# Optimization experiments

Measured on AMD Instinct MI355X. Metric: run time of the kernel, lower is better.

## Reference

```python
import jax, jax.numpy as jnp
import numpy as np

B, T, C = 2, 2048, 2048
H, HKV, D = 16, 4, 128
GROUPS = H // HKV  # num_key_value_groups
EPS = 1e-6


def setup_inputs() -> dict:
    key = jax.random.key(0)
    ks = jax.random.split(key, 6)
    s = 0.02
    return {
        "hidden_states": jax.random.normal(ks[0], (B, T, C), jnp.float32),
        "Wq": jax.random.normal(ks[1], (C, H * D), jnp.float32) * s,
        "Wk": jax.random.normal(ks[2], (C, HKV * D), jnp.float32) * s,
        "Wv": jax.random.normal(ks[3], (C, HKV * D), jnp.float32) * s,
        "Wo": jax.random.normal(ks[4], (H * D, C), jnp.float32) * s,
        "keep_mask": jax.random.randint(ks[5], (T,), 0, 2) > 0,
    }


def reference(hidden_states, Wq, Wk, Wv, Wo, keep_mask):
    # Base attention (standard causal GQA attention with output_attentions=True)
    q = (hidden_states @ Wq).reshape(B, T, H, D).transpose(0, 2, 1, 3)      # [B,H,T,D]
    k = (hidden_states @ Wk).reshape(B, T, HKV, D).transpose(0, 2, 1, 3)    # [B,Hkv,S,D]
    v = (hidden_states @ Wv).reshape(B, T, HKV, D).transpose(0, 2, 1, 3)    # [B,Hkv,S,D]
    k_rep = jnp.repeat(k, GROUPS, axis=1)                                    # [B,H,S,D]
    v_rep = jnp.repeat(v, GROUPS, axis=1)                                    # [B,H,S,D]
    scale = 1.0 / jnp.sqrt(jnp.float32(D))
    scores = jnp.einsum("bhtd,bhsd->bhts", q, k_rep) * scale                 # [B,H,T,S]
    causal = jnp.tril(jnp.ones((T, T), dtype=bool))
    scores = jnp.where(causal[None, None], scores, jnp.float32(-1e9))
    attn_w = jax.nn.softmax(scores, axis=-1)                                 # [B,H,T,S]

    # ScratchpadPrunedAttention: mask dropped positions, renormalize,
    # recompute context and o_proj.
    keep = keep_mask.astype(attn_w.dtype)[None, None, None, :]               # [1,1,1,S]
    attn_w = attn_w * keep
    attn_w = attn_w / (attn_w.sum(-1, keepdims=True) + EPS)
    new_ctx = jnp.einsum("bhts,bhsd->bhtd", attn_w, v_rep)                   # [B,H,T,D]
    new_ctx = new_ctx.transpose(0, 2, 1, 3).reshape(B, T, H * D)             # [B,T,H*D]
    out = new_ctx @ Wo                                                        # [B,T,C]
    return out, attn_w
```

## Files before the change

### kernel.cpp

```cpp
#include <hip/hip_runtime.h>
#include <hip/hip_bf16.h>
#include <stdint.h>

#define B_ 2
#define T_ 2048
#define C_ 2048
#define H_ 16
#define HKV_ 4
#define D_ 128
#define M_ (B_*T_)
static constexpr float SCL = 0.08838834764831845f * 1.4426950408889634f;
static constexpr float EPS_ = 1e-6f;

typedef short bf16x8 __attribute__((ext_vector_type(8)));
typedef float f32x4 __attribute__((ext_vector_type(4)));

__device__ __forceinline__ f32x4 zero4() {
  f32x4 v; v[0] = 0.f; v[1] = 0.f; v[2] = 0.f; v[3] = 0.f; return v;
}

__device__ __forceinline__ unsigned short f2bf(float x) {
  union { float f; unsigned u; } v; v.f = x;
  unsigned r = (v.u + 0x7FFFu + ((v.u >> 16) & 1u)) >> 16;
  return (unsigned short)r;
}

__device__ __forceinline__ void gl_lds16(const void* g, void* l) {
  __builtin_amdgcn_global_load_lds((const __attribute__((address_space(1))) void*)g,
                                   (__attribute__((address_space(3))) void*)l, 16, 0, 0);
}

__global__ void k_cvt(const float* __restrict__ in, unsigned short* __restrict__ out, int n) {
  int i = (blockIdx.x * blockDim.x + threadIdx.x) * 8;
  int stride = gridDim.x * blockDim.x * 8;
  for (; i < n; i += stride) {
    float4 a = *(const float4*)(in + i);
    float4 b = *(const float4*)(in + i + 4);
    ushort4 o0; o0.x = f2bf(a.x); o0.y = f2bf(a.y); o0.z = f2bf(a.z); o0.w = f2bf(a.w);
    ushort4 o1; o1.x = f2bf(b.x); o1.y = f2bf(b.y); o1.z = f2bf(b.z); o1.w = f2bf(b.w);
    *(ushort4*)(out + i) = o0;
    *(ushort4*)(out + i + 4) = o1;
  }
}

__global__ void k_cvt_t(const float* __restrict__ in, unsigned short* __restrict__ out,
                        int R, int Cc) {
  __shared__ float ld[32][33];
  int c0 = blockIdx.x * 32, r0 = blockIdx.y * 32;
  int x = threadIdx.x, y = threadIdx.y;
#pragma unroll
  for (int i = 0; i < 4; i++)
    ld[y * 4 + i][x] = in[(size_t)(r0 + y * 4 + i) * Cc + c0 + x];
  __syncthreads();
#pragma unroll
  for (int i = 0; i < 4; i++)
    out[(size_t)(c0 + y * 4 + i) * R + r0 + x] = f2bf(ld[x][y * 4 + i]);
}

template <int WRITE_F32>
__global__ __launch_bounds__(256) void k_gemm(const unsigned short* __restrict__ A,
                                              const unsigned short* __restrict__ Bt,
                                              void* __restrict__ Cout,
                                              int Mdim, int Ndim, int K) {
  __shared__ __align__(16) unsigned short As[128 * 64];
  __shared__ __align__(16) unsigned short Bs[128 * 64];
  const int tid = threadIdx.x;
  const int wid = tid >> 6, lane = tid & 63;
  const int wm = wid >> 1, wn = wid & 1;
  const int m0 = blockIdx.y * 128, n0 = blockIdx.x * 128;
  const int lrow = tid >> 3, lcol = (tid & 7) * 8;
  const int g = lane >> 4, lr = lane & 15;

  f32x4 acc[4][4];
#pragma unroll
  for (int i = 0; i < 4; i++)
#pragma unroll
    for (int j = 0; j < 4; j++) acc[i][j] = zero4();

  for (int k0 = 0; k0 < K; k0 += 64) {
    __syncthreads();
#pragma unroll
    for (int it = 0; it < 4; it++) {
      gl_lds16(A + (size_t)(m0 + lrow + it * 32) * K + k0 + lcol, (void*)(As + tid * 8 + it * 2048));
      gl_lds16(Bt + (size_t)(n0 + lrow + it * 32) * K + k0 + lcol, (void*)(Bs + tid * 8 + it * 2048));
    }
    __syncthreads();
#pragma unroll
    for (int kk = 0; kk < 2; kk++) {
      bf16x8 af[4], bfr[4];
#pragma unroll
      for (int i = 0; i < 4; i++)
        af[i] = *(const bf16x8*)(As + (wm * 64 + i * 16 + lr) * 64 + kk * 32 + g * 8);
#pragma unroll
      for (int j = 0; j < 4; j++)
        bfr[j] = *(const bf16x8*)(Bs + (wn * 64 + j * 16 + lr) * 64 + kk * 32 + g * 8);
#pragma unroll
      for (int i = 0; i < 4; i++)
#pragma unroll
        for (int j = 0; j < 4; j++)
          acc[i][j] = __builtin_amdgcn_mfma_f32_16x16x32_bf16(af[i], bfr[j], acc[i][j], 0, 0, 0);
    }
  }

#pragma unroll
  for (int i = 0; i < 4; i++)
#pragma unroll
    for (int j = 0; j < 4; j++)
#pragma unroll
      for (int r = 0; r < 4; r++) {
        int row = m0 + wm * 64 + i * 16 + g * 4 + r;
        int col = n0 + wn * 64 + j * 16 + lr;
        if (WRITE_F32)
          ((float*)Cout)[(size_t)row * Ndim + col] = acc[i][j][r];
        else
          ((unsigned short*)Cout)[(size_t)row * Ndim + col] = f2bf(acc[i][j][r]);
      }
}

__global__ __launch_bounds__(256) void k_attn(const unsigned short* __restrict__ qb,
                                              const unsigned short* __restrict__ kb,
                                              const unsigned short* __restrict__ vt,
                                              const int* __restrict__ mask,
                                              float* __restrict__ attn,
                                              unsigned short* __restrict__ ctx)
{
  __shared__ __align__(16) unsigned short Ks[2][64 * 128];
  __shared__ __align__(16) unsigned short Vs[2][128 * 64];
  __shared__ __align__(16) unsigned short Ps[4][16 * 64];
  __shared__ float keeps[2048];

  const int tid = threadIdx.x;
  const int wid = tid >> 6, lane = tid & 63;
  const int g = lane >> 4, lr = lane & 15;
  const int lr7 = lr & 7;
  const int qt = 31 - blockIdx.y;
  const int bh = blockIdx.x;
  const int b = bh >> 4, h = bh & 15, hkv = h >> 2;
  const int qbase = qt * 64;

  const unsigned short* qp = qb + (size_t)(b * T_ + qbase) * 2048 + h * 128;
  const unsigned short* kp = kb + (size_t)(b * T_) * 512 + hkv * 128;
  const unsigned short* vp = vt + (size_t)(hkv * 128) * 4096 + b * T_;
  float* ap = attn + (size_t)(bh * T_ + qbase) * 2048;
  unsigned short* cp = ctx + (size_t)(b * T_ + qbase) * 2048 + h * 128;

#pragma unroll
  for (int i = 0; i < 8; i++)
    keeps[tid * 8 + i] = (mask[tid * 8 + i] != 0) ? 1.0f : 0.0f;

  bf16x8 qa[4];
#pragma unroll
  for (int ks = 0; ks < 4; ks++)
    qa[ks] = *(const bf16x8*)(qp + (size_t)(wid * 16 + lr) * 2048 + ks * 32 + g * 8);

  const int srow = tid >> 4;
  const int scolb = ((tid & 15) * 16) ^ ((srow & 7) << 4);
  const int vrow = tid >> 3;
  const int vcolb = ((tid & 7) * 16) ^ ((vrow & 7) << 4);

  auto stageK = [&](int st, int bufi) {
    const unsigned short* src = kp + (size_t)(st * 64 + srow) * 512 + (scolb >> 1);
    unsigned short* dst = Ks[bufi] + tid * 8;
#pragma unroll
    for (int it = 0; it < 4; it++)
      gl_lds16(src + (size_t)it * 16 * 512, (void*)(dst + it * 2048));
  };
  auto stageV = [&](int st, int bufi) {
    const unsigned short* src = vp + (size_t)vrow * 4096 + st * 64 + (vcolb >> 1);
    unsigned short* dst = Vs[bufi] + tid * 8;
#pragma unroll
    for (int it = 0; it < 4; it++)
      gl_lds16(src + (size_t)it * 32 * 4096, (void*)(dst + it * 2048));
  };

  float z[4] = {0, 0, 0, 0}, zk[4] = {0, 0, 0, 0};

  stageK(0, 0);
  asm volatile("s_waitcnt vmcnt(0) lgkmcnt(0)" ::: "memory");
  __builtin_amdgcn_s_barrier();
  for (int st = 0; st <= qt; st++) {
    const int cur = st & 1;
    if (st < qt) stageK(st + 1, cur ^ 1);
    const unsigned short* kt = Ks[cur];
#pragma unroll
    for (int j = 0; j < 4; j++) {
      f32x4 sc = zero4();
      const unsigned short* kbase = kt + (j * 16 + lr) * 128;
#pragma unroll
      for (int ks = 0; ks < 4; ks++) {
        bf16x8 kf = *(const bf16x8*)(kbase + (((ks * 64 + g * 16) ^ (lr7 << 4)) >> 1));
        sc = __builtin_amdgcn_mfma_f32_16x16x32_bf16(qa[ks], kf, sc, 0, 0, 0);
      }
      int sg = st * 64 + j * 16 + lr;
      float kpv = keeps[sg];
#pragma unroll
      for (int r = 0; r < 4; r++) {
        int tg = qbase + wid * 16 + g * 4 + r;
        float e = (sg <= tg) ? __builtin_amdgcn_exp2f(sc[r] * SCL) : 0.0f;
        z[r] += e;
        zk[r] += e * kpv;
      }
    }
    asm volatile("s_waitcnt vmcnt(0)" ::: "memory");
    __builtin_amdgcn_s_barrier();
  }

  stageK(qt, 0);
  stageV(qt, 0);
#pragma unroll
  for (int r = 0; r < 4; r++) {
#pragma unroll
    for (int m = 1; m < 16; m <<= 1) {
      z[r] += __shfl_xor(z[r], m);
      zk[r] += __shfl_xor(zk[r], m);
    }
  }
  float inv[4];
#pragma unroll
  for (int r = 0; r < 4; r++) inv[r] = 1.0f / (zk[r] + EPS_ * z[r]);

  f32x4 cacc[8];
#pragma unroll
  for (int n = 0; n < 8; n++) cacc[n] = zero4();

  asm volatile("s_waitcnt vmcnt(0)" ::: "memory");
  __builtin_amdgcn_s_barrier();

  for (int st = qt; st >= 0; st--) {
    const int cur = (qt - st) & 1;
    if (st > 0) { stageK(st - 1, cur ^ 1); stageV(st - 1, cur ^ 1); }
    __builtin_amdgcn_sched_barrier(0);
    const int s0 = st * 64;
    const unsigned short* kt = Ks[cur];
    const unsigned short* vtile = Vs[cur];
#pragma unroll
    for (int j = 0; j < 4; j++) {
      f32x4 sc = zero4();
      const unsigned short* kbase = kt + (j * 16 + lr) * 128;
#pragma unroll
      for (int ks = 0; ks < 4; ks++) {
        bf16x8 kf = *(const bf16x8*)(kbase + (((ks * 64 + g * 16) ^ (lr7 << 4)) >> 1));
        sc = __builtin_amdgcn_mfma_f32_16x16x32_bf16(qa[ks], kf, sc, 0, 0, 0);
      }
      int sg = s0 + j * 16 + lr;
      float kpv = keeps[sg];
#pragma unroll
      for (int r = 0; r < 4; r++) {
        int row = wid * 16 + g * 4 + r;
        int tg = qbase + row;
        float e = (sg <= tg) ? __builtin_amdgcn_exp2f(sc[r] * SCL) : 0.0f;
        float a = e * kpv * inv[r];
        ap[(size_t)row * 2048 + sg] = a;
        int prow = g * 4 + r;
        Ps[wid][prow * 64 + (((j * 32 + lr * 2) ^ ((prow & 7) << 4)) >> 1)] = f2bf(a);
      }
    }
    asm volatile("s_waitcnt lgkmcnt(0)" ::: "memory");
    __builtin_amdgcn_sched_barrier(0);
#pragma unroll
    for (int kk = 0; kk < 2; kk++) {
      bf16x8 pa = *(const bf16x8*)(&Ps[wid][lr * 64 + (((kk * 64 + g * 16) ^ (lr7 << 4)) >> 1)]);
#pragma unroll
      for (int n = 0; n < 8; n++) {
        bf16x8 vf = *(const bf16x8*)(vtile + (n * 16 + lr) * 64 + (((kk * 64 + g * 16) ^ (lr7 << 4)) >> 1));
        cacc[n] = __builtin_amdgcn_mfma_f32_16x16x32_bf16(pa, vf, cacc[n], 0, 0, 0);
      }
    }
    asm volatile("s_waitcnt vmcnt(16)" ::: "memory");
    __builtin_amdgcn_s_barrier();
  }

#pragma unroll
  for (int n = 0; n < 8; n++)
#pragma unroll
    for (int r = 0; r < 4; r++)
      cp[(size_t)(wid * 16 + g * 4 + r) * 2048 + n * 16 + lr] = f2bf(cacc[n][r]);

  const int zc0 = qbase + 64;
  if (zc0 < 2048) {
    float4 zf; zf.x = 0.f; zf.y = 0.f; zf.z = 0.f; zf.w = 0.f;
    float* aprow = ap + (size_t)(tid >> 2) * 2048;
    for (int c = zc0 + (tid & 3) * 4; c < 2048; c += 16)
      *(float4*)(aprow + c) = zf;
  }
}

extern "C" void kernel_launch(void* const* d_in, const int* in_sizes, int n_in,
                              void* d_out, int out_size, void* d_ws, size_t ws_size,
                              hipStream_t stream) {
  const float* hs = (const float*)d_in[0];
  const float* Wq = (const float*)d_in[1];
  const float* Wk = (const float*)d_in[2];
  const float* Wv = (const float*)d_in[3];
  const float* Wo = (const float*)d_in[4];
  const int* mask = (const int*)d_in[5];

  char* w = (char*)d_ws;
  unsigned short* hsb = (unsigned short*)w; w += (size_t)M_ * C_ * 2;
  unsigned short* Wqt = (unsigned short*)w; w += (size_t)2048 * 2048 * 2;
  unsigned short* Wkt = (unsigned short*)w; w += (size_t)512 * 2048 * 2;
  unsigned short* Wvt = (unsigned short*)w; w += (size_t)512 * 2048 * 2;
  unsigned short* Wot = (unsigned short*)w; w += (size_t)2048 * 2048 * 2;
  unsigned short* qbuf = (unsigned short*)w; w += (size_t)M_ * 2048 * 2;
  unsigned short* kbuf = (unsigned short*)w; w += (size_t)M_ * 512 * 2;
  unsigned short* vtb = (unsigned short*)w; w += (size_t)512 * M_ * 2;
  unsigned short* ctxb = (unsigned short*)w; w += (size_t)M_ * 2048 * 2;

  float* out = (float*)d_out;
  float* attn = out + (size_t)M_ * C_;

  k_cvt<<<2048, 256, 0, stream>>>(hs, hsb, M_ * C_);
  k_cvt_t<<<dim3(2048 / 32, 2048 / 32), dim3(32, 8), 0, stream>>>(Wq, Wqt, 2048, 2048);
  k_cvt_t<<<dim3(512 / 32, 2048 / 32), dim3(32, 8), 0, stream>>>(Wk, Wkt, 2048, 512);
  k_cvt_t<<<dim3(512 / 32, 2048 / 32), dim3(32, 8), 0, stream>>>(Wv, Wvt, 2048, 512);
  k_cvt_t<<<dim3(2048 / 32, 2048 / 32), dim3(32, 8), 0, stream>>>(Wo, Wot, 2048, 2048);

  k_gemm<0><<<dim3(2048 / 128, 4096 / 128), 256, 0, stream>>>(hsb, Wqt, qbuf, 4096, 2048, 2048);
  k_gemm<0><<<dim3(512 / 128, 4096 / 128), 256, 0, stream>>>(hsb, Wkt, kbuf, 4096, 512, 2048);
  k_gemm<0><<<dim3(4096 / 128, 512 / 128), 256, 0, stream>>>(Wvt, hsb, vtb, 512, 4096, 2048);

  k_attn<<<dim3(32, 32), 256, 0, stream>>>(qbuf, kbuf, vtb, mask, attn, ctxb);

  k_gemm<1><<<dim3(2048 / 128, 4096 / 128), 256, 0, stream>>>(ctxb, Wot, out, 4096, 2048, 2048);
}
```

Measured before the change: 462.9 us.

## Halve attention KV tile to 32, pack keep mask into bits, raise occupancy

Shrinks the attention kernel's K/V staging tiles from 64 to 32 keys, which cuts LDS use so more blocks fit per CU, and adds a launch bound of 4 blocks per CU. The per-block float keep array in LDS is replaced by a tiny pre-kernel that packs the mask into 32-bit words, read per tile. s_setprio hints are placed around the MFMA sections and the vmcnt wait is adjusted to the smaller staging count. In exchange there are twice as many loop iterations and barriers per block, plus one extra tiny kernel launch.

```diff
diff --git a/kernel.cpp b/kernel.cpp
--- a/kernel.cpp
+++ b/kernel.cpp
@@ -55,6 +55,16 @@
 #pragma unroll
   for (int i = 0; i < 4; i++)
     out[(size_t)(c0 + y * 4 + i) * R + r0 + x] = f2bf(ld[x][y * 4 + i]);
+}
+
+__global__ void k_maskbits(const int* __restrict__ mask, unsigned int* __restrict__ mb) {
+  int t = threadIdx.x;
+  if (t < 64) {
+    unsigned int w = 0;
+    for (int b = 0; b < 32; b++)
+      if (mask[t * 32 + b] != 0) w |= (1u << b);
+    mb[t] = w;
+  }
 }
 
 template <int WRITE_F32>
@@ -117,26 +127,26 @@
       }
 }
 
-__global__ __launch_bounds__(256) void k_attn(const unsigned short* __restrict__ qb,
-                                              const unsigned short* __restrict__ kb,
-                                              const unsigned short* __restrict__ vt,
-                                              const int* __restrict__ mask,
-                                              float* __restrict__ attn,
-                                              unsigned short* __restrict__ ctx)
+__global__ __launch_bounds__(256, 4) void k_attn(const unsigned short* __restrict__ qb,
+                                                 const unsigned short* __restrict__ kb,
+                                                 const unsigned short* __restrict__ vt,
+                                                 const unsigned int* __restrict__ mb,
+                                                 float* __restrict__ attn,
+                                                 unsigned short* __restrict__ ctx)
 {
-  __shared__ __align__(16) unsigned short Ks[2][64 * 128];
-  __shared__ __align__(16) unsigned short Vs[2][128 * 64];
-  __shared__ __align__(16) unsigned short Ps[4][16 * 64];
-  __shared__ float keeps[2048];
+  __shared__ __align__(16) unsigned short Ks[2][32 * 128];
+  __shared__ __align__(16) unsigned short Vs[2][128 * 32];
+  __shared__ __align__(16) unsigned short Ps[4][16 * 32];
 
   const int tid = threadIdx.x;
   const int wid = tid >> 6, lane = tid & 63;
   const int g = lane >> 4, lr = lane & 15;
-  const int lr7 = lr & 7;
+  const int lr7 = lr & 7, lr3 = lr & 3;
   const int qt = 31 - blockIdx.y;
   const int bh = blockIdx.x;
   const int b = bh >> 4, h = bh & 15, hkv = h >> 2;
   const int qbase = qt * 64;
+  const int ntile = 2 * qt + 2;
 
   const unsigned short* qp = qb + (size_t)(b * T_ + qbase) * 2048 + h * 128;
   const unsigned short* kp = kb + (size_t)(b * T_) * 512 + hkv * 128;
@@ -144,10 +154,6 @@
   float* ap = attn + (size_t)(bh * T_ + qbase) * 2048;
   unsigned short* cp = ctx + (size_t)(b * T_ + qbase) * 2048 + h * 128;
 
-#pragma unroll
-  for (int i = 0; i < 8; i++)
-    keeps[tid * 8 + i] = (mask[tid * 8 + i] != 0) ? 1.0f : 0.0f;
-
   bf16x8 qa[4];
 #pragma unroll
   for (int ks = 0; ks < 4; ks++)
@@ -155,22 +161,22 @@
 
   const int srow = tid >> 4;
   const int scolb = ((tid & 15) * 16) ^ ((srow & 7) << 4);
-  const int vrow = tid >> 3;
-  const int vcolb = ((tid & 7) * 16) ^ ((vrow & 7) << 4);
+  const int vrow = tid >> 2;
+  const int vcolb = ((tid & 3) * 16) ^ ((vrow & 3) << 4);
 
   auto stageK = [&](int st, int bufi) {
-    const unsigned short* src = kp + (size_t)(st * 64 + srow) * 512 + (scolb >> 1);
+    const unsigned short* src = kp + (size_t)(st * 32 + srow) * 512 + (scolb >> 1);
     unsigned short* dst = Ks[bufi] + tid * 8;
 #pragma unroll
-    for (int it = 0; it < 4; it++)
+    for (int it = 0; it < 2; it++)
       gl_lds16(src + (size_t)it * 16 * 512, (void*)(dst + it * 2048));
   };
   auto stageV = [&](int st, int bufi) {
-    const unsigned short* src = vp + (size_t)vrow * 4096 + st * 64 + (vcolb >> 1);
+    const unsigned short* src = vp + (size_t)vrow * 4096 + st * 32 + (vcolb >> 1);
     unsigned short* dst = Vs[bufi] + tid * 8;
 #pragma unroll
-    for (int it = 0; it < 4; it++)
-      gl_lds16(src + (size_t)it * 32 * 4096, (void*)(dst + it * 2048));
+    for (int it = 0; it < 2; it++)
+      gl_lds16(src + (size_t)it * 64 * 4096, (void*)(dst + it * 2048));
   };
 
   float z[4] = {0, 0, 0, 0}, zk[4] = {0, 0, 0, 0};
@@ -178,21 +184,24 @@
   stageK(0, 0);
   asm volatile("s_waitcnt vmcnt(0) lgkmcnt(0)" ::: "memory");
   __builtin_amdgcn_s_barrier();
-  for (int st = 0; st <= qt; st++) {
+  for (int st = 0; st < ntile; st++) {
     const int cur = st & 1;
-    if (st < qt) stageK(st + 1, cur ^ 1);
+    if (st + 1 < ntile) stageK(st + 1, cur ^ 1);
     const unsigned short* kt = Ks[cur];
 #pragma unroll
-    for (int j = 0; j < 4; j++) {
+    for (int j = 0; j < 2; j++) {
       f32x4 sc = zero4();
       const unsigned short* kbase = kt + (j * 16 + lr) * 128;
+      __builtin_amdgcn_s_setprio(1);
 #pragma unroll
       for (int ks = 0; ks < 4; ks++) {
         bf16x8 kf = *(const bf16x8*)(kbase + (((ks * 64 + g * 16) ^ (lr7 << 4)) >> 1));
         sc = __builtin_amdgcn_mfma_f32_16x16x32_bf16(qa[ks], kf, sc, 0, 0, 0);
       }
-      int sg = st * 64 + j * 16 + lr;
-      float kpv = keeps[sg];
+      __builtin_amdgcn_s_setprio(0);
+      int sg = st * 32 + j * 16 + lr;
+      unsigned int w = mb[st];
+      float kpv = (float)((w >> (j * 16 + lr)) & 1u);
 #pragma unroll
       for (int r = 0; r < 4; r++) {
         int tg = qbase + wid * 16 + g * 4 + r;
@@ -205,8 +214,8 @@
     __builtin_amdgcn_s_barrier();
   }
 
-  stageK(qt, 0);
-  stageV(qt, 0);
+  stageK(ntile - 1, 0);
+  stageV(ntile - 1, 0);
 #pragma unroll
   for (int r = 0; r < 4; r++) {
 #pragma unroll
@@ -226,24 +235,27 @@
   asm volatile("s_waitcnt vmcnt(0)" ::: "memory");
   __builtin_amdgcn_s_barrier();
 
-  for (int st = qt; st >= 0; st--) {
-    const int cur = (qt - st) & 1;
+  for (int st = ntile - 1; st >= 0; st--) {
+    const int cur = (ntile - 1 - st) & 1;
     if (st > 0) { stageK(st - 1, cur ^ 1); stageV(st - 1, cur ^ 1); }
     __builtin_amdgcn_sched_barrier(0);
-    const int s0 = st * 64;
+    const int s0 = st * 32;
     const unsigned short* kt = Ks[cur];
     const unsigned short* vtile = Vs[cur];
-#pragma unroll
-    for (int j = 0; j < 4; j++) {
+    unsigned int w = mb[st];
+#pragma unroll
+    for (int j = 0; j < 2; j++) {
       f32x4 sc = zero4();
       const unsigned short* kbase = kt + (j * 16 + lr) * 128;
+      __builtin_amdgcn_s_setprio(1);
 #pragma unroll
       for (int ks = 0; ks < 4; ks++) {
         bf16x8 kf = *(const bf16x8*)(kbase + (((ks * 64 + g * 16) ^ (lr7 << 4)) >> 1));
         sc = __builtin_amdgcn_mfma_f32_16x16x32_bf16(qa[ks], kf, sc, 0, 0, 0);
       }
+      __builtin_amdgcn_s_setprio(0);
       int sg = s0 + j * 16 + lr;
-      float kpv = keeps[sg];
+      float kpv = (float)((w >> (j * 16 + lr)) & 1u);
 #pragma unroll
       for (int r = 0; r < 4; r++) {
         int row = wid * 16 + g * 4 + r;
@@ -252,21 +264,23 @@
         float a = e * kpv * inv[r];
         ap[(size_t)row * 2048 + sg] = a;
         int prow = g * 4 + r;
-        Ps[wid][prow * 64 + (((j * 32 + lr * 2) ^ ((prow & 7) << 4)) >> 1)] = f2bf(a);
+        Ps[wid][prow * 32 + (((j * 32 + lr * 2) ^ ((prow & 3) << 4)) >> 1)] = f2bf(a);
       }
     }
     asm volatile("s_waitcnt lgkmcnt(0)" ::: "memory");
     __builtin_amdgcn_sched_barrier(0);
-#pragma unroll
-    for (int kk = 0; kk < 2; kk++) {
-      bf16x8 pa = *(const bf16x8*)(&Ps[wid][lr * 64 + (((kk * 64 + g * 16) ^ (lr7 << 4)) >> 1)]);
+    {
+      bf16x8 pa = *(const bf16x8*)(&Ps[wid][lr * 32 + (((g * 16) ^ (lr3 << 4)) >> 1)]);
+      __builtin_amdgcn_s_setprio(1);
 #pragma unroll
       for (int n = 0; n < 8; n++) {
-        bf16x8 vf = *(const bf16x8*)(vtile + (n * 16 + lr) * 64 + (((kk * 64 + g * 16) ^ (lr7 << 4)) >> 1));
+        int vrw = n * 16 + lr;
+        bf16x8 vf = *(const bf16x8*)(vtile + vrw * 32 + (((g * 16) ^ ((vrw & 3) << 4)) >> 1));
         cacc[n] = __builtin_amdgcn_mfma_f32_16x16x32_bf16(pa, vf, cacc[n], 0, 0, 0);
       }
-    }
-    asm volatile("s_waitcnt vmcnt(16)" ::: "memory");
+      __builtin_amdgcn_s_setprio(0);
+    }
+    asm volatile("s_waitcnt vmcnt(8)" ::: "memory");
     __builtin_amdgcn_s_barrier();
   }
 
@@ -305,6 +319,7 @@
   unsigned short* kbuf = (unsigned short*)w; w += (size_t)M_ * 512 * 2;
   unsigned short* vtb = (unsigned short*)w; w += (size_t)512 * M_ * 2;
   unsigned short* ctxb = (unsigned short*)w; w += (size_t)M_ * 2048 * 2;
+  unsigned int* mbits = (unsigned int*)w;  w += 256;
 
   float* out = (float*)d_out;
   float* attn = out + (size_t)M_ * C_;
@@ -314,12 +329,13 @@
   k_cvt_t<<<dim3(512 / 32, 2048 / 32), dim3(32, 8), 0, stream>>>(Wk, Wkt, 2048, 512);
   k_cvt_t<<<dim3(512 / 32, 2048 / 32), dim3(32, 8), 0, stream>>>(Wv, Wvt, 2048, 512);
   k_cvt_t<<<dim3(2048 / 32, 2048 / 32), dim3(32, 8), 0, stream>>>(Wo, Wot, 2048, 2048);
+  k_maskbits<<<1, 64, 0, stream>>>(mask, mbits);
 
   k_gemm<0><<<dim3(2048 / 128, 4096 / 128), 256, 0, stream>>>(hsb, Wqt, qbuf, 4096, 2048, 2048);
   k_gemm<0><<<dim3(512 / 128, 4096 / 128), 256, 0, stream>>>(hsb, Wkt, kbuf, 4096, 512, 2048);
   k_gemm<0><<<dim3(4096 / 128, 512 / 128), 256, 0, stream>>>(Wvt, hsb, vtb, 512, 4096, 2048);
 
-  k_attn<<<dim3(32, 32), 256, 0, stream>>>(qbuf, kbuf, vtb, mask, attn, ctxb);
+  k_attn<<<dim3(32, 32), 256, 0, stream>>>(qbuf, kbuf, vtb, mbits, attn, ctxb);
 
   k_gemm<1><<<dim3(2048 / 128, 4096 / 128), 256, 0, stream>>>(ctxb, Wot, out, 4096, 2048, 2048);
 }
```

New measurement: 453.9 us. No clear change (-1.9%).
